# Performance work log

Hardware: AMD Instinct MI355X
Metric: run time of the kernel (lower is better)

The kernel has to match this reference:

```python
import jax, jax.numpy as jnp
import numpy as np

BN_EPS = 1e-5
NORM_EPS = 1e-12  # F.normalize default eps


def reference(x, conv_w, bn_gamma, bn_beta):
    # 1x1 conv dimension reduction: [B,2048,H,W] -> [B,256,H,W]
    z = jnp.einsum('bchw,dc->bdhw', x, conv_w)
    # BatchNorm2d (training-mode batch statistics) + ReLU
    mu = z.mean(axis=(0, 2, 3), keepdims=True)
    var = z.var(axis=(0, 2, 3), keepdims=True)
    z = (z - mu) / jnp.sqrt(var + BN_EPS)
    z = z * bn_gamma.reshape(1, -1, 1, 1) + bn_beta.reshape(1, -1, 1, 1)
    z = jax.nn.relu(z)

    B, d, h, w = z.shape
    M = h * w
    xm = z.reshape(B, d, M)
    # Covpool: y = x I_hat x^T with I_hat = (I - 11^T/M)/M == centered 2nd moment
    xc = xm - xm.mean(axis=-1, keepdims=True)
    cov = jnp.einsum('bdm,bem->bde', xc, xc) / M  # [B,d,d]

    # Eigen decomposition (cov is symmetric PSD; SVD of PSD == eigh)
    s, U = jnp.linalg.eigh(cov)  # s: [B,d], U: [B,d,d]
    eps = jnp.finfo(cov.dtype).eps
    s = jnp.maximum(s, eps)

    # ExponentialInverse: U exp(-S) U^T
    inv_x = jnp.einsum('bid,bd,bjd->bij', U, jnp.exp(-s), U)
    # Power (matrix sqrt): U S^{1/2} U^T
    out = jnp.einsum('bid,bd,bjd->bij', U, jnp.sqrt(s), U)

    # attention = out @ inv_x^T  (inv_x is symmetric, transpose kept for fidelity)
    att = jnp.einsum('bij,bkj->bik', out, inv_x)
    flat = att.reshape(B, -1)
    nrm = jnp.maximum(jnp.linalg.norm(flat, axis=1, keepdims=True), NORM_EPS)
    normalized = (flat / nrm).reshape(att.shape)
    att = out * (att / normalized)

    y = att + out
    iu = jnp.triu_indices(d)
    return y[:, iu[0], iu[1]]  # [B, d*(d+1)/2]


def setup_inputs() -> dict:
    key = jax.random.key(0)
    k1, k2 = jax.random.split(key)
    x = jax.random.normal(k1, (32, 2048, 28, 28), dtype=jnp.float32)
    # kaiming-normal fan_out scaling for 1x1 conv: std = sqrt(2/fan_out)=sqrt(2/256)
    conv_w = jax.random.normal(k2, (256, 2048), dtype=jnp.float32) * np.sqrt(2.0 / 256.0)
    bn_gamma = jnp.ones((256,), dtype=jnp.float32)
    bn_beta = jnp.zeros((256,), dtype=jnp.float32)
    return {'x': x, 'conv_w': conv_w, 'bn_gamma': bn_gamma, 'bn_beta': bn_beta}
```

## Files before the change

kernel.cpp:

```cpp
#include <hip/hip_runtime.h>


typedef unsigned short u16;
typedef __attribute__((ext_vector_type(8))) short bf16x8;
typedef __attribute__((ext_vector_type(4))) float f32x4;

__device__ __forceinline__ u16 f2bf(float f) {
  unsigned u = __builtin_bit_cast(unsigned, f);
  u += 0x7FFFu + ((u >> 16) & 1u);
  return (u16)(u >> 16);
}
__device__ __forceinline__ float bf2f(u16 h) {
  unsigned u = ((unsigned)h) << 16;
  return __builtin_bit_cast(float, u);
}

__device__ __forceinline__
void mm_core(const u16* __restrict__ Ah, const u16* __restrict__ Al,
             const u16* __restrict__ Bh, const u16* __restrict__ Bl,
             long boff, int row0, int col0,
             u16 (*lds)[128][8][8], f32x4 acc[4][4])
{
  const int tid = threadIdx.x;
  const int wave = tid >> 6, lane = tid & 63;
  const int wm = wave >> 1, wn = wave & 1;
  const int mL = lane & 15, q = lane >> 4;
  const u16* baseA[2] = {Ah + boff, Al + boff};
  const u16* baseB[2] = {Bh + boff, Bl + boff};

  for (int k0 = 0; k0 < 256; k0 += 64) {
    __syncthreads();
#pragma unroll
    for (int it = 0; it < 16; ++it) {
      const int t = it >> 2;
      const int r = ((it & 3) << 8) + tid;
      const int m = r >> 3, c = r & 7;
      const u16* src = (t < 2 ? baseA[t] : baseB[t - 2])
                     + (long)((t < 2 ? row0 : col0) + m) * 256 + k0 + c * 8;
      const uint4 v = *reinterpret_cast<const uint4*>(src);
      *reinterpret_cast<uint4*>(&lds[t][m][c ^ (m & 7)][0]) = v;
    }
    __syncthreads();
#pragma unroll
    for (int kk = 0; kk < 2; ++kk) {
      bf16x8 ah[4], al[4], bh[4], bl[4];
#pragma unroll
      for (int i = 0; i < 4; ++i) {
        const int ma = wm * 64 + i * 16 + mL;
        const int ca = (kk * 4 + q) ^ (ma & 7);
        ah[i] = *reinterpret_cast<const bf16x8*>(&lds[0][ma][ca][0]);
        al[i] = *reinterpret_cast<const bf16x8*>(&lds[1][ma][ca][0]);
        const int nb = wn * 64 + i * 16 + mL;
        const int cb = (kk * 4 + q) ^ (nb & 7);
        bh[i] = *reinterpret_cast<const bf16x8*>(&lds[2][nb][cb][0]);
        bl[i] = *reinterpret_cast<const bf16x8*>(&lds[3][nb][cb][0]);
      }
#pragma unroll
      for (int i = 0; i < 4; ++i)
#pragma unroll
        for (int j = 0; j < 4; ++j) {
          acc[i][j] = __builtin_amdgcn_mfma_f32_16x16x32_bf16(ah[i], bh[j], acc[i][j], 0, 0, 0);
          acc[i][j] = __builtin_amdgcn_mfma_f32_16x16x32_bf16(ah[i], bl[j], acc[i][j], 0, 0, 0);
          acc[i][j] = __builtin_amdgcn_mfma_f32_16x16x32_bf16(al[i], bh[j], acc[i][j], 0, 0, 0);
        }
    }
  }
}

template<int MB>
__global__ __launch_bounds__(256)
void fuse_k(const u16* __restrict__ A0, const u16* __restrict__ B0, u16* __restrict__ C0,
            float al0, float b10, float dg0, const float* __restrict__ cf0,
            const u16* __restrict__ A1, const u16* __restrict__ B1, u16* __restrict__ C1,
            u16* __restrict__ D1, float al1, float b11, float dg1,
            float hc1, float hc2, float hc3, const float* __restrict__ cf1, long LO)
{
  __shared__ u16 lds[4][128][8][8];
  int z = blockIdx.z;
  const bool hB = (z >= 32);
  const u16 *Ah, *Bh; u16 *C, *D = nullptr;
  float al, b1, dg; const float* cf;
  if (!hB) { Ah = A0; Bh = B0; C = C0; al = al0; b1 = b10; dg = dg0; cf = cf0; }
  else { z -= 32; Ah = A1; Bh = B1; C = C1; D = D1; al = al1; b1 = b11; dg = dg1; cf = cf1; }
  const long boff = (long)z * 65536;
  const int row0 = blockIdx.y * 128, col0 = blockIdx.x * 128;
  const int wave = threadIdx.x >> 6, lane = threadIdx.x & 63;
  const int wm = wave >> 1, wn = wave & 1;
  const int mL = lane & 15, q = lane >> 4;

  f32x4 acc[4][4];
#pragma unroll
  for (int i = 0; i < 4; ++i)
#pragma unroll
    for (int j = 0; j < 4; ++j) acc[i][j] = {0.f, 0.f, 0.f, 0.f};

  mm_core(Ah, Ah + LO, Bh, Bh + LO, boff, row0, col0, lds, acc);

#pragma unroll
  for (int i = 0; i < 4; ++i) {
    const int rbase = row0 + wm * 64 + i * 16 + q * 4;
#pragma unroll
    for (int j = 0; j < 4; ++j) {
      const int cc = col0 + wn * 64 + j * 16 + mL;
#pragma unroll
      for (int rg = 0; rg < 4; ++rg) {
        const int rr = rbase + rg;
        const long o = boff + (long)rr * 256 + cc;
        const float vr = acc[i][j][rg];
        if (MB == 1 && hB) {
          u16 h = f2bf(vr);
          C[o] = h; C[o + LO] = f2bf(vr - bf2f(h));
          float hv = fmaf(vr, hc1, cf[o] * hc2);
          if (rr == cc) hv += hc3;
          h = f2bf(hv);
          D[o] = h; D[o + LO] = f2bf(hv - bf2f(h));
        } else {
          float v = al * vr;
          if (cf) v = fmaf(b1, cf[o], v);
          if (rr == cc) v += dg;
          const u16 h = f2bf(v);
          C[o] = h; C[o + LO] = f2bf(v - bf2f(h));
        }
      }
    }
  }
}

__global__ __launch_bounds__(256)
void gemm2_pair_k(const u16* __restrict__ A0, const u16* __restrict__ B0, u16* __restrict__ C0,
                  const u16* __restrict__ A1, const u16* __restrict__ B1, u16* __restrict__ C1,
                  long LO)
{
  __shared__ u16 lds[4][128][8][8];
  int z = blockIdx.z;
  const u16 *Ah, *Bh; u16* Chp;
  if (z < 32) { Ah = A0; Bh = B0; Chp = C0; }
  else { z -= 32; Ah = A1; Bh = B1; Chp = C1; }
  const long boff = (long)z * 65536;
  const int row0 = blockIdx.y * 128, col0 = blockIdx.x * 128;
  const int wave = threadIdx.x >> 6, lane = threadIdx.x & 63;
  const int wm = wave >> 1, wn = wave & 1;
  const int mL = lane & 15, q = lane >> 4;

  f32x4 acc[4][4];
#pragma unroll
  for (int i = 0; i < 4; ++i)
#pragma unroll
    for (int j = 0; j < 4; ++j) acc[i][j] = {0.f, 0.f, 0.f, 0.f};

  mm_core(Ah, Ah + LO, Bh, Bh + LO, boff, row0, col0, lds, acc);

#pragma unroll
  for (int i = 0; i < 4; ++i) {
    const int rbase = row0 + wm * 64 + i * 16 + q * 4;
#pragma unroll
    for (int j = 0; j < 4; ++j) {
      const int cc = col0 + wn * 64 + j * 16 + mL;
#pragma unroll
      for (int rg = 0; rg < 4; ++rg) {
        const long o = boff + (long)(rbase + rg) * 256 + cc;
        const float v = acc[i][j][rg];
        const u16 h = f2bf(v);
        Chp[o] = h; Chp[o + LO] = f2bf(v - bf2f(h));
      }
    }
  }
}

template<int MODE>
__global__ __launch_bounds__(256)
void gemmN64_k(const u16* __restrict__ Ah, const u16* __restrict__ Al,
               const u16* __restrict__ Bh, const u16* __restrict__ Bl,
               u16* __restrict__ Ch, u16* __restrict__ Cl,
               const float* __restrict__ cf, float alpha, float b1, float diag,
               float* __restrict__ attn2)
{
  __shared__ u16 ldsA[2][128][8][8];
  __shared__ u16 ldsB[2][64][8][8];
  const long boff = (long)blockIdx.z * 65536;
  const int row0 = blockIdx.y * 128, col0 = blockIdx.x * 64;
  const int tid = threadIdx.x;
  const int wave = tid >> 6, lane = tid & 63;
  const int wm = wave >> 1, wn = wave & 1;
  const int mL = lane & 15, q = lane >> 4;
  const u16* baseA[2] = {Ah + boff, Al + boff};
  const u16* baseB[2] = {Bh + boff, Bl + boff};

  f32x4 acc[4][2];
#pragma unroll
  for (int i = 0; i < 4; ++i)
#pragma unroll
    for (int j = 0; j < 2; ++j) acc[i][j] = {0.f, 0.f, 0.f, 0.f};

  for (int k0 = 0; k0 < 256; k0 += 64) {
    __syncthreads();
#pragma unroll
    for (int it = 0; it < 8; ++it) {
      const int t = it >> 2;
      const int r = ((it & 3) << 8) + tid;
      const int m = r >> 3, c = r & 7;
      const uint4 v = *reinterpret_cast<const uint4*>(
          baseA[t] + (long)(row0 + m) * 256 + k0 + c * 8);
      *reinterpret_cast<uint4*>(&ldsA[t][m][c ^ (m & 7)][0]) = v;
    }
#pragma unroll
    for (int it = 0; it < 4; ++it) {
      const int t = it >> 1;
      const int r = ((it & 1) << 8) + tid;
      const int m = r >> 3, c = r & 7;
      const uint4 v = *reinterpret_cast<const uint4*>(
          baseB[t] + (long)(col0 + m) * 256 + k0 + c * 8);
      *reinterpret_cast<uint4*>(&ldsB[t][m][c ^ (m & 7)][0]) = v;
    }
    __syncthreads();
#pragma unroll
    for (int kk = 0; kk < 2; ++kk) {
      bf16x8 ah[4], alo[4], bh[2], bl[2];
#pragma unroll
      for (int i = 0; i < 4; ++i) {
        const int ma = wm * 64 + i * 16 + mL;
        const int ca = (kk * 4 + q) ^ (ma & 7);
        ah[i]  = *reinterpret_cast<const bf16x8*>(&ldsA[0][ma][ca][0]);
        alo[i] = *reinterpret_cast<const bf16x8*>(&ldsA[1][ma][ca][0]);
      }
#pragma unroll
      for (int j = 0; j < 2; ++j) {
        const int nb = wn * 32 + j * 16 + mL;
        const int cb = (kk * 4 + q) ^ (nb & 7);
        bh[j] = *reinterpret_cast<const bf16x8*>(&ldsB[0][nb][cb][0]);
        bl[j] = *reinterpret_cast<const bf16x8*>(&ldsB[1][nb][cb][0]);
      }
#pragma unroll
      for (int i = 0; i < 4; ++i)
#pragma unroll
        for (int j = 0; j < 2; ++j) {
          acc[i][j] = __builtin_amdgcn_mfma_f32_16x16x32_bf16(ah[i],  bh[j], acc[i][j], 0, 0, 0);
          acc[i][j] = __builtin_amdgcn_mfma_f32_16x16x32_bf16(ah[i],  bl[j], acc[i][j], 0, 0, 0);
          acc[i][j] = __builtin_amdgcn_mfma_f32_16x16x32_bf16(alo[i], bh[j], acc[i][j], 0, 0, 0);
        }
    }
  }

  if (MODE == 2) {
    float ssum = 0.f;
#pragma unroll
    for (int i = 0; i < 4; ++i)
#pragma unroll
      for (int j = 0; j < 2; ++j)
#pragma unroll
        for (int rg = 0; rg < 4; ++rg) ssum = fmaf(acc[i][j][rg], acc[i][j][rg], ssum);
#pragma unroll
    for (int o = 32; o > 0; o >>= 1) ssum += __shfl_down(ssum, o);
    __syncthreads();
    float* red = (float*)&ldsA[0][0][0][0];
    if (lane == 0) red[wave] = ssum;
    __syncthreads();
    if (tid == 0)
      atomicAdd(attn2 + blockIdx.z, red[0] + red[1] + red[2] + red[3]);
    return;
  }

#pragma unroll
  for (int i = 0; i < 4; ++i) {
    const int rbase = row0 + wm * 64 + i * 16 + q * 4;
#pragma unroll
    for (int j = 0; j < 2; ++j) {
      const int cc = col0 + wn * 32 + j * 16 + mL;
#pragma unroll
      for (int rg = 0; rg < 4; ++rg) {
        const int rr = rbase + rg;
        const long o = boff + (long)rr * 256 + cc;
        float v = alpha * acc[i][j][rg];
        if (cf) v = fmaf(b1, cf[o], v);
        if (rr == cc) v += diag;
        const u16 h = f2bf(v);
        Ch[o] = h; Cl[o] = f2bf(v - bf2f(h));
      }
    }
  }
}

__global__ __launch_bounds__(256)
void conv_k(const u16* __restrict__ wb, const float* __restrict__ x,
            float* __restrict__ z0, float* __restrict__ z1)
{
  __shared__ u16 ldsA[64][8][8];
  __shared__ u16 ldsB[128][8][8];
  const int tid = threadIdx.x;
  const int b = blockIdx.z;
  const int n0 = blockIdx.x * 128;
  const int m0 = (blockIdx.y & 3) * 64;
  const int ks = blockIdx.y >> 2;
  const int kb0 = ks * 1024;
  const int wave = tid >> 6, lane = tid & 63;
  const int wm = wave >> 1, wn = wave & 1;
  const int mL = lane & 15, q = lane >> 4;
  const float* xb = x + (long)b * 2048 * 784;
  float* zp = (ks == 0 ? z0 : z1);

  f32x4 acc[2][4];
#pragma unroll
  for (int i = 0; i < 2; ++i)
#pragma unroll
    for (int j = 0; j < 4; ++j) acc[i][j] = {0.f, 0.f, 0.f, 0.f};

  const int kc = tid >> 5, nc = tid & 31;
  const int nbase = nc * 4;
  const int gn = n0 + nbase;

  for (int k0 = 0; k0 < 1024; k0 += 64) {
    const int kg = kb0 + k0;
    __syncthreads();
#pragma unroll
    for (int it = 0; it < 2; ++it) {
      const int g = it * 256 + tid;
      const int m = g >> 3, c = g & 7;
      const uint4 v = *reinterpret_cast<const uint4*>(
          wb + (long)(m0 + m) * 2048 + kg + c * 8);
      *reinterpret_cast<uint4*>(&ldsA[m][c ^ (m & 7)][0]) = v;
    }
    {
      float vv[8][4];
#pragma unroll
      for (int jk = 0; jk < 8; ++jk) {
        float4 f = make_float4(0.f, 0.f, 0.f, 0.f);
        if (gn < 784)
          f = *reinterpret_cast<const float4*>(xb + (long)(kg + kc * 8 + jk) * 784 + gn);
        vv[jk][0] = f.x; vv[jk][1] = f.y; vv[jk][2] = f.z; vv[jk][3] = f.w;
      }
#pragma unroll
      for (int jn = 0; jn < 4; ++jn) {
        const int n = nbase + jn;
        const int ch = kc ^ (n & 7);
        ushort4 ua, ub;
        ua.x = f2bf(vv[0][jn]); ua.y = f2bf(vv[1][jn]);
        ua.z = f2bf(vv[2][jn]); ua.w = f2bf(vv[3][jn]);
        ub.x = f2bf(vv[4][jn]); ub.y = f2bf(vv[5][jn]);
        ub.z = f2bf(vv[6][jn]); ub.w = f2bf(vv[7][jn]);
        *reinterpret_cast<ushort4*>(&ldsB[n][ch][0]) = ua;
        *reinterpret_cast<ushort4*>(&ldsB[n][ch][4]) = ub;
      }
    }
    __syncthreads();
#pragma unroll
    for (int kk = 0; kk < 2; ++kk) {
      bf16x8 af[2], bfv[4];
#pragma unroll
      for (int i = 0; i < 2; ++i) {
        const int ma = wm * 32 + i * 16 + mL;
        af[i] = *reinterpret_cast<const bf16x8*>(&ldsA[ma][(kk * 4 + q) ^ (ma & 7)][0]);
      }
#pragma unroll
      for (int j = 0; j < 4; ++j) {
        const int nb = wn * 64 + j * 16 + mL;
        bfv[j] = *reinterpret_cast<const bf16x8*>(&ldsB[nb][(kk * 4 + q) ^ (nb & 7)][0]);
      }
#pragma unroll
      for (int i = 0; i < 2; ++i)
#pragma unroll
        for (int j = 0; j < 4; ++j)
          acc[i][j] = __builtin_amdgcn_mfma_f32_16x16x32_bf16(af[i], bfv[j], acc[i][j], 0, 0, 0);
    }
  }
#pragma unroll
  for (int i = 0; i < 2; ++i) {
    const int rbase = m0 + wm * 32 + i * 16 + q * 4;
#pragma unroll
    for (int j = 0; j < 4; ++j) {
      const int cc = n0 + wn * 64 + j * 16 + mL;
      if (cc >= 784) continue;
#pragma unroll
      for (int rg = 0; rg < 4; ++rg)
        zp[((long)b * 256 + rbase + rg) * 784 + cc] = acc[i][j][rg];
    }
  }
}

__global__ __launch_bounds__(256)
void gram_k(const u16* __restrict__ zb, const float* __restrict__ rs,
            float* __restrict__ cov, u16* __restrict__ C2h, u16* __restrict__ C2l)
{
  __shared__ u16 lds[2][128][8][8];
  const int tid = threadIdx.x;
  const int b = blockIdx.z;
  const int col0 = blockIdx.x * 128, row0 = blockIdx.y * 128;
  const int wave = tid >> 6, lane = tid & 63;
  const int wm = wave >> 1, wn = wave & 1;
  const int mL = lane & 15, q = lane >> 4;
  const u16* zbb = zb + (long)b * 256 * 832;

  f32x4 acc[4][4];
#pragma unroll
  for (int i = 0; i < 4; ++i)
#pragma unroll
    for (int j = 0; j < 4; ++j) acc[i][j] = {0.f, 0.f, 0.f, 0.f};

  for (int k0 = 0; k0 < 832; k0 += 64) {
    __syncthreads();
#pragma unroll
    for (int it = 0; it < 8; ++it) {
      const int t = it >> 2;
      const int r = ((it & 3) << 8) + tid;
      const int m = r >> 3, c = r & 7;
      const int grow = (t == 0 ? row0 : col0) + m;
      const uint4 v = *reinterpret_cast<const uint4*>(zbb + (long)grow * 832 + k0 + c * 8);
      *reinterpret_cast<uint4*>(&lds[t][m][c ^ (m & 7)][0]) = v;
    }
    __syncthreads();
#pragma unroll
    for (int kk = 0; kk < 2; ++kk) {
      bf16x8 af[4], bfv[4];
#pragma unroll
      for (int i = 0; i < 4; ++i) {
        const int ma = wm * 64 + i * 16 + mL;
        af[i] = *reinterpret_cast<const bf16x8*>(&lds[0][ma][(kk * 4 + q) ^ (ma & 7)][0]);
        const int nb = wn * 64 + i * 16 + mL;
        bfv[i] = *reinterpret_cast<const bf16x8*>(&lds[1][nb][(kk * 4 + q) ^ (nb & 7)][0]);
      }
#pragma unroll
      for (int i = 0; i < 4; ++i)
#pragma unroll
        for (int j = 0; j < 4; ++j)
          acc[i][j] = __builtin_amdgcn_mfma_f32_16x16x32_bf16(af[i], bfv[j], acc[i][j], 0, 0, 0);
    }
  }
  const float inv_m = 1.f / 784.f;
#pragma unroll
  for (int i = 0; i < 4; ++i) {
    const int rr0 = row0 + wm * 64 + i * 16 + q * 4;
#pragma unroll
    for (int j = 0; j < 4; ++j) {
      const int cc = col0 + wn * 64 + j * 16 + mL;
      const float mu_c = rs[b * 256 + cc] * inv_m;
#pragma unroll
      for (int rg = 0; rg < 4; ++rg) {
        const int rr = rr0 + rg;
        const float mu_r = rs[b * 256 + rr] * inv_m;
        const long o = ((long)b * 256 + rr) * 256 + cc;
        const float cv = fmaf(acc[i][j][rg], inv_m, -mu_r * mu_c);
        cov[o] = cv;
        const u16 h = f2bf(cv);
        C2h[o] = h; C2l[o] = f2bf(cv - bf2f(h));
      }
    }
  }
}

__global__ __launch_bounds__(256)
void bn_stats_k(const float* __restrict__ z0, const float* __restrict__ z1,
                float* __restrict__ ps, float* __restrict__ pq)
{
  const int d = blockIdx.x, sl = blockIdx.y, t = threadIdx.x;
  const int lane = t & 63, wid = t >> 6;
  __shared__ float ws[4], wq[4];
  float s = 0.f, qq = 0.f;
  for (int b = sl * 4; b < sl * 4 + 4; ++b) {
    const long off = ((long)b * 256 + d) * 784;
    for (int m = t; m < 784; m += 256) {
      const float v = z0[off + m] + z1[off + m];
      s += v; qq = fmaf(v, v, qq);
    }
  }
#pragma unroll
  for (int o = 32; o > 0; o >>= 1) { s += __shfl_down(s, o); qq += __shfl_down(qq, o); }
  if (lane == 0) { ws[wid] = s; wq[wid] = qq; }
  __syncthreads();
  if (t == 0) {
    ps[d * 8 + sl] = ws[0] + ws[1] + ws[2] + ws[3];
    pq[d * 8 + sl] = wq[0] + wq[1] + wq[2] + wq[3];
  }
}

__global__ __launch_bounds__(256)
void bn_apply_k(const float* __restrict__ z0, const float* __restrict__ z1,
                const float* __restrict__ gamma, const float* __restrict__ beta,
                const float* __restrict__ ps, const float* __restrict__ pq,
                u16* __restrict__ zb, float* __restrict__ rs)
{
  const int d = blockIdx.x, b = blockIdx.y, t = threadIdx.x;
  const int lane = t & 63, wid = t >> 6;
  __shared__ float bc[2], ws[4];
  if (t == 0) {
    float sum = 0.f, sq = 0.f;
#pragma unroll
    for (int s8 = 0; s8 < 8; ++s8) { sum += ps[d * 8 + s8]; sq += pq[d * 8 + s8]; }
    const float inv_n = 1.f / 25088.f;
    const float mean = sum * inv_n;
    const float var = sq * inv_n - mean * mean;
    const float sc = gamma[d] * rsqrtf(var + 1e-5f);
    bc[0] = sc; bc[1] = fmaf(-mean, sc, beta[d]);
  }
  __syncthreads();
  const float sc = bc[0], sh = bc[1];
  const long off = ((long)b * 256 + d) * 784;
  u16* qp = zb + ((long)b * 256 + d) * 832;
  float rsum = 0.f;
  for (int m = t; m < 832; m += 256) {
    const float v = (m < 784)
        ? fmaxf(fmaf(z0[off + m] + z1[off + m], sc, sh), 0.f) : 0.f;
    qp[m] = f2bf(v);
    rsum += v;
  }
#pragma unroll
  for (int o = 32; o > 0; o >>= 1) rsum += __shfl_down(rsum, o);
  if (lane == 0) ws[wid] = rsum;
  __syncthreads();
  if (t == 0) rs[b * 256 + d] = ws[0] + ws[1] + ws[2] + ws[3];
}

__global__ __launch_bounds__(1024)
void power_k(const float* __restrict__ cov, float* __restrict__ s,
             float* __restrict__ attn2)
{
  const int b = blockIdx.x, tid = threadIdx.x;
  const int i = tid & 255, g = tid >> 8;
  const float* A = cov + (long)b * 65536;
  __shared__ float v[256];
  __shared__ float part[4][256];
  __shared__ float red[4];
  if (g == 0) v[i] = 1.f;
  __syncthreads();
  float lam = 1.f;
  for (int it = 0; it < 10; ++it) {
    float u = 0.f;
    const int jb = g * 64;
#pragma unroll 8
    for (int j = jb; j < jb + 64; ++j) u = fmaf(A[(long)j * 256 + i], v[j], u);
    part[g][i] = u;
    __syncthreads();
    if (g == 0) {
      u = part[0][i] + part[1][i] + part[2][i] + part[3][i];
      float ss = u * u;
#pragma unroll
      for (int o = 32; o > 0; o >>= 1) ss += __shfl_down(ss, o);
      if ((i & 63) == 0) red[i >> 6] = ss;
    }
    __syncthreads();
    lam = sqrtf(red[0] + red[1] + red[2] + red[3]);
    if (g == 0) v[i] = u / lam;
    __syncthreads();
  }
  if (tid == 0) { s[b] = 1.8f / lam; attn2[b] = 0.f; }
}

__global__ __launch_bounds__(256)
void init_k(const float* __restrict__ cov, const float* __restrict__ s,
            u16* __restrict__ Yh, u16* __restrict__ Yl,
            u16* __restrict__ Th, u16* __restrict__ Tl)
{
  const int b = blockIdx.y, i = blockIdx.x, j = threadIdx.x;
  const long o = ((long)b * 256 + i) * 256 + j;
  const float a = cov[o] * s[b];
  u16 h = f2bf(a);
  Yh[o] = h; Yl[o] = f2bf(a - bf2f(h));
  float tv = -0.5f * a;
  if (i == j) tv += 1.5f;
  h = f2bf(tv);
  Th[o] = h; Tl[o] = f2bf(tv - bf2f(h));
}

__global__ __launch_bounds__(256)
void out_k(const u16* __restrict__ Yh, const u16* __restrict__ Yl,
           const float* __restrict__ s, const float* __restrict__ attn2,
           float* __restrict__ out)
{
  const int i = blockIdx.x, b = blockIdx.y, j = threadIdx.x;
  if (j < i) return;
  const float inv = rsqrtf(s[b]);
  const float nrm = fmaxf(sqrtf(fmaxf(attn2[b], 0.f)) * inv, 1e-12f);
  const float scv = inv * (1.f + nrm);
  const long o = ((long)b * 256 + i) * 256 + j;
  const long off = (long)b * 32896 + (long)i * 256 - (long)i * (i - 1) / 2 + (j - i);
  out[off] = (bf2f(Yh[o]) + bf2f(Yl[o])) * scv;
}

__global__ __launch_bounds__(256)
void cast_w_k(const float* __restrict__ w, u16* __restrict__ wb)
{
  const int idx = blockIdx.x * 256 + threadIdx.x;
  wb[idx] = f2bf(w[idx]);
}

extern "C" void kernel_launch(void* const* d_in, const int* in_sizes, int n_in,
                              void* d_out, int out_size, void* d_ws, size_t ws_size,
                              hipStream_t stream)
{
  const float* x     = (const float*)d_in[0];
  const float* w     = (const float*)d_in[1];
  const float* gamma = (const float*)d_in[2];
  const float* beta  = (const float*)d_in[3];
  float* out = (float*)d_out;

  const long PS = 4194304;
  const long LO = 2097152;
  u16* S[9];
  for (int k = 0; k < 9; ++k) S[k] = (u16*)d_ws + (long)k * PS;
  char* base = (char*)d_ws;
  float* z0  = (float*)(base + 75497472);
  float* z1  = (float*)(base + 101187584);
  u16*   zb  = (u16*)(base + 126877696);
  float* cov = (float*)(base + 140509184);
  u16*   wbuf = (u16*)(base + 140509184);
  float* st  = (float*)(base + 148897792);
  float* sv = st, *attn2 = st + 32, *rs = st + 64;
  float* ps = st + 64 + 8192, *pq = ps + 2048;
  u16 *C2 = S[5], *V = S[6], *Ha = S[7], *Hb = S[8];

  const dim3 blk(256);
  const dim3 gP(2, 2, 64);
  const dim3 gT(4, 2, 32);
  const dim3 gE(256, 32);

  cast_w_k<<<dim3(2048), blk, 0, stream>>>(w, wbuf);
  conv_k<<<dim3(7, 8, 32), blk, 0, stream>>>(wbuf, x, z0, z1);
  bn_stats_k<<<dim3(256, 8), blk, 0, stream>>>(z0, z1, ps, pq);
  bn_apply_k<<<dim3(256, 32), blk, 0, stream>>>(z0, z1, gamma, beta, ps, pq, zb, rs);
  gram_k<<<dim3(2, 2, 32), blk, 0, stream>>>(zb, rs, cov, C2, C2 + LO);
  power_k<<<dim3(32), dim3(1024), 0, stream>>>(cov, sv, attn2);
  init_k<<<gE, blk, 0, stream>>>(cov, sv, S[0], S[0] + LO, S[1], S[1] + LO);

  fuse_k<1><<<gP, blk, 0, stream>>>(
      S[0], S[1], S[2], 1.f, 0.f, 0.f, (const float*)nullptr,
      C2, C2, V, Ha, 1.f, 0.f, 0.f,
      1.f / 40320.f, -1.f / 5040.f, 1.f / 720.f, cov, LO);

  int iY = 2, iZ = 1, fa = 0, fb = 3, fc = 4;
  for (int it = 1; it <= 7; ++it) {
    const int iT = fa;
    if (it == 1)
      fuse_k<0><<<gP, blk, 0, stream>>>(
          S[iZ], S[iY], S[iT], -0.5f, 0.f, 1.5f, (const float*)nullptr,
          V, Ha, Hb, (u16*)nullptr, 1.f, -1.f / 120.f, 1.f / 24.f,
          0.f, 0.f, 0.f, cov, LO);
    else if (it == 2)
      fuse_k<0><<<gP, blk, 0, stream>>>(
          S[iZ], S[iY], S[iT], -0.5f, 0.f, 1.5f, (const float*)nullptr,
          V, Hb, Ha, (u16*)nullptr, 1.f, -1.f / 6.f, 0.5f,
          0.f, 0.f, 0.f, cov, LO);
    else if (it == 3)
      fuse_k<0><<<gP, blk, 0, stream>>>(
          S[iZ], S[iY], S[iT], -0.5f, 0.f, 1.5f, (const float*)nullptr,
          V, Ha, Hb, (u16*)nullptr, 1.f, -1.f, 1.f,
          0.f, 0.f, 0.f, cov, LO);
    else
      gemmN64_k<0><<<gT, blk, 0, stream>>>(
          S[iZ], S[iZ] + LO, S[iY], S[iY] + LO, S[iT], S[iT] + LO,
          (const float*)nullptr, -0.5f, 0.f, 1.5f, (float*)nullptr);
    if (it < 7) {
      gemm2_pair_k<<<gP, blk, 0, stream>>>(S[iY], S[iT], S[fb],
                                           S[iT], S[iZ], S[fc], LO);
      const int nY = fb, nZ = fc;
      fa = iY; fb = iZ; fc = iT;
      iY = nY; iZ = nZ;
    } else {
      gemmN64_k<0><<<gT, blk, 0, stream>>>(
          S[iY], S[iY] + LO, S[iT], S[iT] + LO, S[fb], S[fb] + LO,
          (const float*)nullptr, 1.f, 0.f, 0.f, (float*)nullptr);
      iY = fb;
    }
  }

  gemmN64_k<2><<<gT, blk, 0, stream>>>(
      S[iY], S[iY] + LO, Hb, Hb + LO, (u16*)nullptr, (u16*)nullptr,
      (const float*)nullptr, 1.f, 0.f, 0.f, attn2);
  out_k<<<gE, blk, 0, stream>>>(S[iY], S[iY] + LO, sv, attn2, out);
}
```

Before: 742.7 us.

## Use 512-thread blocks across GEMM kernels and retile conv to full-M tiles

Moves the GEMM kernels (fuse, pair, N64, gram) from 4 to 8 waves per block, halving the per-wave output tile so there are more waves to hide latency on these small batched 256x256 products. The gram kernel changes to 128x64 tiles on a larger grid. The conv kernel is retiled so each block covers all 256 output channels over 64 spatial columns, loading x with scalar coalesced reads instead of float4 and reusing each x tile across every output channel. In exchange, per-wave operand reuse from LDS drops and the conv path loses its vectorized global loads.

```diff
diff --git a/kernel.cpp b/kernel.cpp
--- a/kernel.cpp
+++ b/kernel.cpp
@@ -19,11 +19,11 @@
 void mm_core(const u16* __restrict__ Ah, const u16* __restrict__ Al,
              const u16* __restrict__ Bh, const u16* __restrict__ Bl,
              long boff, int row0, int col0,
-             u16 (*lds)[128][8][8], f32x4 acc[4][4])
+             u16 (*lds)[128][8][8], f32x4 acc[4][2])
 {
   const int tid = threadIdx.x;
   const int wave = tid >> 6, lane = tid & 63;
-  const int wm = wave >> 1, wn = wave & 1;
+  const int wm = wave >> 2, wn = wave & 3;
   const int mL = lane & 15, q = lane >> 4;
   const u16* baseA[2] = {Ah + boff, Al + boff};
   const u16* baseB[2] = {Bh + boff, Bl + boff};
@@ -31,34 +31,37 @@
   for (int k0 = 0; k0 < 256; k0 += 64) {
     __syncthreads();
 #pragma unroll
-    for (int it = 0; it < 16; ++it) {
-      const int t = it >> 2;
-      const int r = ((it & 3) << 8) + tid;
+    for (int it = 0; it < 8; ++it) {
+      const int t = it >> 1;
+      const int r = ((it & 1) << 9) + tid;
       const int m = r >> 3, c = r & 7;
       const u16* src = (t < 2 ? baseA[t] : baseB[t - 2])
                      + (long)((t < 2 ? row0 : col0) + m) * 256 + k0 + c * 8;
-      const uint4 v = *reinterpret_cast<const uint4*>(src);
-      *reinterpret_cast<uint4*>(&lds[t][m][c ^ (m & 7)][0]) = v;
+      *reinterpret_cast<uint4*>(&lds[t][m][c ^ (m & 7)][0]) =
+          *reinterpret_cast<const uint4*>(src);
     }
     __syncthreads();
 #pragma unroll
     for (int kk = 0; kk < 2; ++kk) {
-      bf16x8 ah[4], al[4], bh[4], bl[4];
+      bf16x8 ah[4], al[4], bh[2], bl[2];
 #pragma unroll
       for (int i = 0; i < 4; ++i) {
         const int ma = wm * 64 + i * 16 + mL;
         const int ca = (kk * 4 + q) ^ (ma & 7);
         ah[i] = *reinterpret_cast<const bf16x8*>(&lds[0][ma][ca][0]);
         al[i] = *reinterpret_cast<const bf16x8*>(&lds[1][ma][ca][0]);
-        const int nb = wn * 64 + i * 16 + mL;
+      }
+#pragma unroll
+      for (int j = 0; j < 2; ++j) {
+        const int nb = wn * 32 + j * 16 + mL;
         const int cb = (kk * 4 + q) ^ (nb & 7);
-        bh[i] = *reinterpret_cast<const bf16x8*>(&lds[2][nb][cb][0]);
-        bl[i] = *reinterpret_cast<const bf16x8*>(&lds[3][nb][cb][0]);
+        bh[j] = *reinterpret_cast<const bf16x8*>(&lds[2][nb][cb][0]);
+        bl[j] = *reinterpret_cast<const bf16x8*>(&lds[3][nb][cb][0]);
       }
 #pragma unroll
       for (int i = 0; i < 4; ++i)
 #pragma unroll
-        for (int j = 0; j < 4; ++j) {
+        for (int j = 0; j < 2; ++j) {
           acc[i][j] = __builtin_amdgcn_mfma_f32_16x16x32_bf16(ah[i], bh[j], acc[i][j], 0, 0, 0);
           acc[i][j] = __builtin_amdgcn_mfma_f32_16x16x32_bf16(ah[i], bl[j], acc[i][j], 0, 0, 0);
           acc[i][j] = __builtin_amdgcn_mfma_f32_16x16x32_bf16(al[i], bh[j], acc[i][j], 0, 0, 0);
@@ -68,7 +71,7 @@
 }
 
 template<int MB>
-__global__ __launch_bounds__(256)
+__global__ __launch_bounds__(512)
 void fuse_k(const u16* __restrict__ A0, const u16* __restrict__ B0, u16* __restrict__ C0,
             float al0, float b10, float dg0, const float* __restrict__ cf0,
             const u16* __restrict__ A1, const u16* __restrict__ B1, u16* __restrict__ C1,
@@ -85,14 +88,14 @@
   const long boff = (long)z * 65536;
   const int row0 = blockIdx.y * 128, col0 = blockIdx.x * 128;
   const int wave = threadIdx.x >> 6, lane = threadIdx.x & 63;
-  const int wm = wave >> 1, wn = wave & 1;
+  const int wm = wave >> 2, wn = wave & 3;
   const int mL = lane & 15, q = lane >> 4;
 
-  f32x4 acc[4][4];
+  f32x4 acc[4][2];
 #pragma unroll
   for (int i = 0; i < 4; ++i)
 #pragma unroll
-    for (int j = 0; j < 4; ++j) acc[i][j] = {0.f, 0.f, 0.f, 0.f};
+    for (int j = 0; j < 2; ++j) acc[i][j] = {0.f, 0.f, 0.f, 0.f};
 
   mm_core(Ah, Ah + LO, Bh, Bh + LO, boff, row0, col0, lds, acc);
 
@@ -100,8 +103,8 @@
   for (int i = 0; i < 4; ++i) {
     const int rbase = row0 + wm * 64 + i * 16 + q * 4;
 #pragma unroll
-    for (int j = 0; j < 4; ++j) {
-      const int cc = col0 + wn * 64 + j * 16 + mL;
+    for (int j = 0; j < 2; ++j) {
+      const int cc = col0 + wn * 32 + j * 16 + mL;
 #pragma unroll
       for (int rg = 0; rg < 4; ++rg) {
         const int rr = rbase + rg;
@@ -126,7 +129,7 @@
   }
 }
 
-__global__ __launch_bounds__(256)
+__global__ __launch_bounds__(512)
 void gemm2_pair_k(const u16* __restrict__ A0, const u16* __restrict__ B0, u16* __restrict__ C0,
                   const u16* __restrict__ A1, const u16* __restrict__ B1, u16* __restrict__ C1,
                   long LO)
@@ -139,14 +142,14 @@
   const long boff = (long)z * 65536;
   const int row0 = blockIdx.y * 128, col0 = blockIdx.x * 128;
   const int wave = threadIdx.x >> 6, lane = threadIdx.x & 63;
-  const int wm = wave >> 1, wn = wave & 1;
+  const int wm = wave >> 2, wn = wave & 3;
   const int mL = lane & 15, q = lane >> 4;
 
-  f32x4 acc[4][4];
+  f32x4 acc[4][2];
 #pragma unroll
   for (int i = 0; i < 4; ++i)
 #pragma unroll
-    for (int j = 0; j < 4; ++j) acc[i][j] = {0.f, 0.f, 0.f, 0.f};
+    for (int j = 0; j < 2; ++j) acc[i][j] = {0.f, 0.f, 0.f, 0.f};
 
   mm_core(Ah, Ah + LO, Bh, Bh + LO, boff, row0, col0, lds, acc);
 
@@ -154,8 +157,8 @@
   for (int i = 0; i < 4; ++i) {
     const int rbase = row0 + wm * 64 + i * 16 + q * 4;
 #pragma unroll
-    for (int j = 0; j < 4; ++j) {
-      const int cc = col0 + wn * 64 + j * 16 + mL;
+    for (int j = 0; j < 2; ++j) {
+      const int cc = col0 + wn * 32 + j * 16 + mL;
 #pragma unroll
       for (int rg = 0; rg < 4; ++rg) {
         const long o = boff + (long)(rbase + rg) * 256 + cc;
@@ -168,7 +171,7 @@
 }
 
 template<int MODE>
-__global__ __launch_bounds__(256)
+__global__ __launch_bounds__(512)
 void gemmN64_k(const u16* __restrict__ Ah, const u16* __restrict__ Al,
                const u16* __restrict__ Bh, const u16* __restrict__ Bl,
                u16* __restrict__ Ch, u16* __restrict__ Cl,
@@ -186,39 +189,35 @@
   const u16* baseA[2] = {Ah + boff, Al + boff};
   const u16* baseB[2] = {Bh + boff, Bl + boff};
 
-  f32x4 acc[4][2];
-#pragma unroll
-  for (int i = 0; i < 4; ++i)
+  f32x4 acc[2][2];
+#pragma unroll
+  for (int i = 0; i < 2; ++i)
 #pragma unroll
     for (int j = 0; j < 2; ++j) acc[i][j] = {0.f, 0.f, 0.f, 0.f};
 
   for (int k0 = 0; k0 < 256; k0 += 64) {
     __syncthreads();
-#pragma unroll
-    for (int it = 0; it < 8; ++it) {
-      const int t = it >> 2;
-      const int r = ((it & 3) << 8) + tid;
-      const int m = r >> 3, c = r & 7;
-      const uint4 v = *reinterpret_cast<const uint4*>(
-          baseA[t] + (long)(row0 + m) * 256 + k0 + c * 8);
-      *reinterpret_cast<uint4*>(&ldsA[t][m][c ^ (m & 7)][0]) = v;
-    }
 #pragma unroll
     for (int it = 0; it < 4; ++it) {
       const int t = it >> 1;
-      const int r = ((it & 1) << 8) + tid;
+      const int r = ((it & 1) << 9) + tid;
       const int m = r >> 3, c = r & 7;
-      const uint4 v = *reinterpret_cast<const uint4*>(
-          baseB[t] + (long)(col0 + m) * 256 + k0 + c * 8);
-      *reinterpret_cast<uint4*>(&ldsB[t][m][c ^ (m & 7)][0]) = v;
+      *reinterpret_cast<uint4*>(&ldsA[t][m][c ^ (m & 7)][0]) =
+          *reinterpret_cast<const uint4*>(baseA[t] + (long)(row0 + m) * 256 + k0 + c * 8);
+    }
+#pragma unroll
+    for (int it = 0; it < 2; ++it) {
+      const int m = tid >> 3, c = tid & 7;
+      *reinterpret_cast<uint4*>(&ldsB[it][m][c ^ (m & 7)][0]) =
+          *reinterpret_cast<const uint4*>(baseB[it] + (long)(col0 + m) * 256 + k0 + c * 8);
     }
     __syncthreads();
 #pragma unroll
     for (int kk = 0; kk < 2; ++kk) {
-      bf16x8 ah[4], alo[4], bh[2], bl[2];
-#pragma unroll
-      for (int i = 0; i < 4; ++i) {
-        const int ma = wm * 64 + i * 16 + mL;
+      bf16x8 ah[2], alo[2], bh[2], bl[2];
+#pragma unroll
+      for (int i = 0; i < 2; ++i) {
+        const int ma = wm * 32 + i * 16 + mL;
         const int ca = (kk * 4 + q) ^ (ma & 7);
         ah[i]  = *reinterpret_cast<const bf16x8*>(&ldsA[0][ma][ca][0]);
         alo[i] = *reinterpret_cast<const bf16x8*>(&ldsA[1][ma][ca][0]);
@@ -231,7 +230,7 @@
         bl[j] = *reinterpret_cast<const bf16x8*>(&ldsB[1][nb][cb][0]);
       }
 #pragma unroll
-      for (int i = 0; i < 4; ++i)
+      for (int i = 0; i < 2; ++i)
 #pragma unroll
         for (int j = 0; j < 2; ++j) {
           acc[i][j] = __builtin_amdgcn_mfma_f32_16x16x32_bf16(ah[i],  bh[j], acc[i][j], 0, 0, 0);
@@ -244,7 +243,7 @@
   if (MODE == 2) {
     float ssum = 0.f;
 #pragma unroll
-    for (int i = 0; i < 4; ++i)
+    for (int i = 0; i < 2; ++i)
 #pragma unroll
       for (int j = 0; j < 2; ++j)
 #pragma unroll
@@ -255,14 +254,18 @@
     float* red = (float*)&ldsA[0][0][0][0];
     if (lane == 0) red[wave] = ssum;
     __syncthreads();
-    if (tid == 0)
-      atomicAdd(attn2 + blockIdx.z, red[0] + red[1] + red[2] + red[3]);
+    if (tid == 0) {
+      float t8 = 0.f;
+#pragma unroll
+      for (int wv = 0; wv < 8; ++wv) t8 += red[wv];
+      atomicAdd(attn2 + blockIdx.z, t8);
+    }
     return;
   }
 
 #pragma unroll
-  for (int i = 0; i < 4; ++i) {
-    const int rbase = row0 + wm * 64 + i * 16 + q * 4;
+  for (int i = 0; i < 2; ++i) {
+    const int rbase = row0 + wm * 32 + i * 16 + q * 4;
 #pragma unroll
     for (int j = 0; j < 2; ++j) {
       const int cc = col0 + wn * 32 + j * 16 + mL;
@@ -280,17 +283,16 @@
   }
 }
 
-__global__ __launch_bounds__(256)
+__global__ __launch_bounds__(512)
 void conv_k(const u16* __restrict__ wb, const float* __restrict__ x,
             float* __restrict__ z0, float* __restrict__ z1)
 {
-  __shared__ u16 ldsA[64][8][8];
-  __shared__ u16 ldsB[128][8][8];
+  __shared__ u16 ldsA[256][8][8];
+  __shared__ u16 ldsB[64][8][8];
   const int tid = threadIdx.x;
   const int b = blockIdx.z;
-  const int n0 = blockIdx.x * 128;
-  const int m0 = (blockIdx.y & 3) * 64;
-  const int ks = blockIdx.y >> 2;
+  const int n0 = blockIdx.x * 64;
+  const int ks = blockIdx.y;
   const int kb0 = ks * 1024;
   const int wave = tid >> 6, lane = tid & 63;
   const int wm = wave >> 1, wn = wave & 1;
@@ -298,76 +300,65 @@
   const float* xb = x + (long)b * 2048 * 784;
   float* zp = (ks == 0 ? z0 : z1);
 
-  f32x4 acc[2][4];
-#pragma unroll
-  for (int i = 0; i < 2; ++i)
-#pragma unroll
-    for (int j = 0; j < 4; ++j) acc[i][j] = {0.f, 0.f, 0.f, 0.f};
-
-  const int kc = tid >> 5, nc = tid & 31;
-  const int nbase = nc * 4;
-  const int gn = n0 + nbase;
+  f32x4 acc[4][2];
+#pragma unroll
+  for (int i = 0; i < 4; ++i)
+#pragma unroll
+    for (int j = 0; j < 2; ++j) acc[i][j] = {0.f, 0.f, 0.f, 0.f};
+
+  const int kc = tid >> 6, nc = tid & 63;
+  const int gn = n0 + nc;
+  const bool nok = (gn < 784);
 
   for (int k0 = 0; k0 < 1024; k0 += 64) {
     const int kg = kb0 + k0;
     __syncthreads();
 #pragma unroll
-    for (int it = 0; it < 2; ++it) {
-      const int g = it * 256 + tid;
+    for (int it = 0; it < 4; ++it) {
+      const int g = it * 512 + tid;
       const int m = g >> 3, c = g & 7;
-      const uint4 v = *reinterpret_cast<const uint4*>(
-          wb + (long)(m0 + m) * 2048 + kg + c * 8);
-      *reinterpret_cast<uint4*>(&ldsA[m][c ^ (m & 7)][0]) = v;
+      *reinterpret_cast<uint4*>(&ldsA[m][c ^ (m & 7)][0]) =
+          *reinterpret_cast<const uint4*>(wb + (long)m * 2048 + kg + c * 8);
     }
     {
-      float vv[8][4];
-#pragma unroll
-      for (int jk = 0; jk < 8; ++jk) {
-        float4 f = make_float4(0.f, 0.f, 0.f, 0.f);
-        if (gn < 784)
-          f = *reinterpret_cast<const float4*>(xb + (long)(kg + kc * 8 + jk) * 784 + gn);
-        vv[jk][0] = f.x; vv[jk][1] = f.y; vv[jk][2] = f.z; vv[jk][3] = f.w;
-      }
-#pragma unroll
-      for (int jn = 0; jn < 4; ++jn) {
-        const int n = nbase + jn;
-        const int ch = kc ^ (n & 7);
-        ushort4 ua, ub;
-        ua.x = f2bf(vv[0][jn]); ua.y = f2bf(vv[1][jn]);
-        ua.z = f2bf(vv[2][jn]); ua.w = f2bf(vv[3][jn]);
-        ub.x = f2bf(vv[4][jn]); ub.y = f2bf(vv[5][jn]);
-        ub.z = f2bf(vv[6][jn]); ub.w = f2bf(vv[7][jn]);
-        *reinterpret_cast<ushort4*>(&ldsB[n][ch][0]) = ua;
-        *reinterpret_cast<ushort4*>(&ldsB[n][ch][4]) = ub;
-      }
+      float vv[8];
+#pragma unroll
+      for (int jk = 0; jk < 8; ++jk)
+        vv[jk] = nok ? xb[(long)(kg + kc * 8 + jk) * 784 + gn] : 0.f;
+      ushort4 ua, ub;
+      ua.x = f2bf(vv[0]); ua.y = f2bf(vv[1]); ua.z = f2bf(vv[2]); ua.w = f2bf(vv[3]);
+      ub.x = f2bf(vv[4]); ub.y = f2bf(vv[5]); ub.z = f2bf(vv[6]); ub.w = f2bf(vv[7]);
+      const int ch = kc ^ (nc & 7);
+      *reinterpret_cast<ushort4*>(&ldsB[nc][ch][0]) = ua;
+      *reinterpret_cast<ushort4*>(&ldsB[nc][ch][4]) = ub;
     }
     __syncthreads();
 #pragma unroll
     for (int kk = 0; kk < 2; ++kk) {
-      bf16x8 af[2], bfv[4];
-#pragma unroll
-      for (int i = 0; i < 2; ++i) {
-        const int ma = wm * 32 + i * 16 + mL;
+      bf16x8 af[4], bfv[2];
+#pragma unroll
+      for (int i = 0; i < 4; ++i) {
+        const int ma = wm * 64 + i * 16 + mL;
         af[i] = *reinterpret_cast<const bf16x8*>(&ldsA[ma][(kk * 4 + q) ^ (ma & 7)][0]);
       }
 #pragma unroll
-      for (int j = 0; j < 4; ++j) {
-        const int nb = wn * 64 + j * 16 + mL;
+      for (int j = 0; j < 2; ++j) {
+        const int nb = wn * 32 + j * 16 + mL;
         bfv[j] = *reinterpret_cast<const bf16x8*>(&ldsB[nb][(kk * 4 + q) ^ (nb & 7)][0]);
       }
 #pragma unroll
-      for (int i = 0; i < 2; ++i)
-#pragma unroll
-        for (int j = 0; j < 4; ++j)
+      for (int i = 0; i < 4; ++i)
+#pragma unroll
+        for (int j = 0; j < 2; ++j)
           acc[i][j] = __builtin_amdgcn_mfma_f32_16x16x32_bf16(af[i], bfv[j], acc[i][j], 0, 0, 0);
     }
   }
 #pragma unroll
-  for (int i = 0; i < 2; ++i) {
-    const int rbase = m0 + wm * 32 + i * 16 + q * 4;
-#pragma unroll
-    for (int j = 0; j < 4; ++j) {
-      const int cc = n0 + wn * 64 + j * 16 + mL;
+  for (int i = 0; i < 4; ++i) {
+    const int rbase = wm * 64 + i * 16 + q * 4;
+#pragma unroll
+    for (int j = 0; j < 2; ++j) {
+      const int cc = n0 + wn * 32 + j * 16 + mL;
       if (cc >= 784) continue;
 #pragma unroll
       for (int rg = 0; rg < 4; ++rg)
@@ -376,61 +367,68 @@
   }
 }
 
-__global__ __launch_bounds__(256)
+__global__ __launch_bounds__(512)
 void gram_k(const u16* __restrict__ zb, const float* __restrict__ rs,
             float* __restrict__ cov, u16* __restrict__ C2h, u16* __restrict__ C2l)
 {
-  __shared__ u16 lds[2][128][8][8];
+  __shared__ u16 ldsA[128][8][8];
+  __shared__ u16 ldsB[64][8][8];
   const int tid = threadIdx.x;
   const int b = blockIdx.z;
-  const int col0 = blockIdx.x * 128, row0 = blockIdx.y * 128;
+  const int col0 = blockIdx.x * 64, row0 = blockIdx.y * 128;
   const int wave = tid >> 6, lane = tid & 63;
   const int wm = wave >> 1, wn = wave & 1;
   const int mL = lane & 15, q = lane >> 4;
   const u16* zbb = zb + (long)b * 256 * 832;
 
-  f32x4 acc[4][4];
-#pragma unroll
-  for (int i = 0; i < 4; ++i)
-#pragma unroll
-    for (int j = 0; j < 4; ++j) acc[i][j] = {0.f, 0.f, 0.f, 0.f};
+  f32x4 acc[2][2];
+#pragma unroll
+  for (int i = 0; i < 2; ++i)
+#pragma unroll
+    for (int j = 0; j < 2; ++j) acc[i][j] = {0.f, 0.f, 0.f, 0.f};
 
   for (int k0 = 0; k0 < 832; k0 += 64) {
     __syncthreads();
 #pragma unroll
-    for (int it = 0; it < 8; ++it) {
-      const int t = it >> 2;
-      const int r = ((it & 3) << 8) + tid;
+    for (int it = 0; it < 2; ++it) {
+      const int r = it * 512 + tid;
       const int m = r >> 3, c = r & 7;
-      const int grow = (t == 0 ? row0 : col0) + m;
-      const uint4 v = *reinterpret_cast<const uint4*>(zbb + (long)grow * 832 + k0 + c * 8);
-      *reinterpret_cast<uint4*>(&lds[t][m][c ^ (m & 7)][0]) = v;
+      *reinterpret_cast<uint4*>(&ldsA[m][c ^ (m & 7)][0]) =
+          *reinterpret_cast<const uint4*>(zbb + (long)(row0 + m) * 832 + k0 + c * 8);
+    }
+    {
+      const int m = tid >> 3, c = tid & 7;
+      *reinterpret_cast<uint4*>(&ldsB[m][c ^ (m & 7)][0]) =
+          *reinterpret_cast<const uint4*>(zbb + (long)(col0 + m) * 832 + k0 + c * 8);
     }
     __syncthreads();
 #pragma unroll
     for (int kk = 0; kk < 2; ++kk) {
-      bf16x8 af[4], bfv[4];
-#pragma unroll
-      for (int i = 0; i < 4; ++i) {
-        const int ma = wm * 64 + i * 16 + mL;
-        af[i] = *reinterpret_cast<const bf16x8*>(&lds[0][ma][(kk * 4 + q) ^ (ma & 7)][0]);
-        const int nb = wn * 64 + i * 16 + mL;
-        bfv[i] = *reinterpret_cast<const bf16x8*>(&lds[1][nb][(kk * 4 + q) ^ (nb & 7)][0]);
-      }
-#pragma unroll
-      for (int i = 0; i < 4; ++i)
-#pragma unroll
-        for (int j = 0; j < 4; ++j)
+      bf16x8 af[2], bfv[2];
+#pragma unroll
+      for (int i = 0; i < 2; ++i) {
+        const int ma = wm * 32 + i * 16 + mL;
+        af[i] = *reinterpret_cast<const bf16x8*>(&ldsA[ma][(kk * 4 + q) ^ (ma & 7)][0]);
+      }
+#pragma unroll
+      for (int j = 0; j < 2; ++j) {
+        const int nb = wn * 32 + j * 16 + mL;
+        bfv[j] = *reinterpret_cast<const bf16x8*>(&ldsB[nb][(kk * 4 + q) ^ (nb & 7)][0]);
+      }
+#pragma unroll
+      for (int i = 0; i < 2; ++i)
+#pragma unroll
+        for (int j = 0; j < 2; ++j)
           acc[i][j] = __builtin_amdgcn_mfma_f32_16x16x32_bf16(af[i], bfv[j], acc[i][j], 0, 0, 0);
     }
   }
   const float inv_m = 1.f / 784.f;
 #pragma unroll
-  for (int i = 0; i < 4; ++i) {
-    const int rr0 = row0 + wm * 64 + i * 16 + q * 4;
-#pragma unroll
-    for (int j = 0; j < 4; ++j) {
-      const int cc = col0 + wn * 64 + j * 16 + mL;
+  for (int i = 0; i < 2; ++i) {
+    const int rr0 = row0 + wm * 32 + i * 16 + q * 4;
+#pragma unroll
+    for (int j = 0; j < 2; ++j) {
+      const int cc = col0 + wn * 32 + j * 16 + mL;
       const float mu_c = rs[b * 256 + cc] * inv_m;
 #pragma unroll
       for (int rg = 0; rg < 4; ++rg) {
@@ -606,20 +604,20 @@
   float* ps = st + 64 + 8192, *pq = ps + 2048;
   u16 *C2 = S[5], *V = S[6], *Ha = S[7], *Hb = S[8];
 
-  const dim3 blk(256);
+  const dim3 blk(256), blk5(512);
   const dim3 gP(2, 2, 64);
   const dim3 gT(4, 2, 32);
   const dim3 gE(256, 32);
 
   cast_w_k<<<dim3(2048), blk, 0, stream>>>(w, wbuf);
-  conv_k<<<dim3(7, 8, 32), blk, 0, stream>>>(wbuf, x, z0, z1);
+  conv_k<<<dim3(13, 2, 32), blk5, 0, stream>>>(wbuf, x, z0, z1);
   bn_stats_k<<<dim3(256, 8), blk, 0, stream>>>(z0, z1, ps, pq);
   bn_apply_k<<<dim3(256, 32), blk, 0, stream>>>(z0, z1, gamma, beta, ps, pq, zb, rs);
-  gram_k<<<dim3(2, 2, 32), blk, 0, stream>>>(zb, rs, cov, C2, C2 + LO);
+  gram_k<<<gT, blk5, 0, stream>>>(zb, rs, cov, C2, C2 + LO);
   power_k<<<dim3(32), dim3(1024), 0, stream>>>(cov, sv, attn2);
   init_k<<<gE, blk, 0, stream>>>(cov, sv, S[0], S[0] + LO, S[1], S[1] + LO);
 
-  fuse_k<1><<<gP, blk, 0, stream>>>(
+  fuse_k<1><<<gP, blk5, 0, stream>>>(
       S[0], S[1], S[2], 1.f, 0.f, 0.f, (const float*)nullptr,
       C2, C2, V, Ha, 1.f, 0.f, 0.f,
       1.f / 40320.f, -1.f / 5040.f, 1.f / 720.f, cov, LO);
@@ -628,39 +626,39 @@
   for (int it = 1; it <= 7; ++it) {
     const int iT = fa;
     if (it == 1)
-      fuse_k<0><<<gP, blk, 0, stream>>>(
+      fuse_k<0><<<gP, blk5, 0, stream>>>(
           S[iZ], S[iY], S[iT], -0.5f, 0.f, 1.5f, (const float*)nullptr,
           V, Ha, Hb, (u16*)nullptr, 1.f, -1.f / 120.f, 1.f / 24.f,
           0.f, 0.f, 0.f, cov, LO);
     else if (it == 2)
-      fuse_k<0><<<gP, blk, 0, stream>>>(
+      fuse_k<0><<<gP, blk5, 0, stream>>>(
           S[iZ], S[iY], S[iT], -0.5f, 0.f, 1.5f, (const float*)nullptr,
           V, Hb, Ha, (u16*)nullptr, 1.f, -1.f / 6.f, 0.5f,
           0.f, 0.f, 0.f, cov, LO);
     else if (it == 3)
-      fuse_k<0><<<gP, blk, 0, stream>>>(
+      fuse_k<0><<<gP, blk5, 0, stream>>>(
           S[iZ], S[iY], S[iT], -0.5f, 0.f, 1.5f, (const float*)nullptr,
           V, Ha, Hb, (u16*)nullptr, 1.f, -1.f, 1.f,
           0.f, 0.f, 0.f, cov, LO);
     else
-      gemmN64_k<0><<<gT, blk, 0, stream>>>(
+      gemmN64_k<0><<<gT, blk5, 0, stream>>>(
           S[iZ], S[iZ] + LO, S[iY], S[iY] + LO, S[iT], S[iT] + LO,
           (const float*)nullptr, -0.5f, 0.f, 1.5f, (float*)nullptr);
     if (it < 7) {
-      gemm2_pair_k<<<gP, blk, 0, stream>>>(S[iY], S[iT], S[fb],
-                                           S[iT], S[iZ], S[fc], LO);
+      gemm2_pair_k<<<gP, blk5, 0, stream>>>(S[iY], S[iT], S[fb],
+                                            S[iT], S[iZ], S[fc], LO);
       const int nY = fb, nZ = fc;
       fa = iY; fb = iZ; fc = iT;
       iY = nY; iZ = nZ;
     } else {
-      gemmN64_k<0><<<gT, blk, 0, stream>>>(
+      gemmN64_k<0><<<gT, blk5, 0, stream>>>(
           S[iY], S[iY] + LO, S[iT], S[iT] + LO, S[fb], S[fb] + LO,
           (const float*)nullptr, 1.f, 0.f, 0.f, (float*)nullptr);
       iY = fb;
     }
   }
 
-  gemmN64_k<2><<<gT, blk, 0, stream>>>(
+  gemmN64_k<2><<<gT, blk5, 0, stream>>>(
       S[iY], S[iY] + LO, Hb, Hb + LO, (u16*)nullptr, (u16*)nullptr,
       (const float*)nullptr, 1.f, 0.f, 0.f, attn2);
   out_k<<<gE, blk, 0, stream>>>(S[iY], S[iY] + LO, sv, attn2, out);
```

New measurement: 681.1 us. 8.3% less time.
